# Kernel optimization log

Measured on AMD Instinct MI355X. Metric: run time of the kernel, lower is better.

Reference implementation:

```python
import jax, jax.numpy as jnp
import numpy as np
import math

N_HEADS = 4
N_KV_GROUPS = 1
HEAD_DIM = 256
SLIDING_WINDOW = 512
ROPE_BASE = 1000000.0
EPS = 1e-6


def _rmsnorm(x, gamma):
    # normalize over last dim (head_dim), torch nn.RMSNorm semantics
    ms = jnp.mean(jnp.square(x), axis=-1, keepdims=True)
    return x * jax.lax.rsqrt(ms + EPS) * gamma


def _rope_tables(T, head_dim, dtype):
    inv_freq = 1.0 / (ROPE_BASE ** (jnp.arange(0, head_dim, 2, dtype=jnp.float32) / head_dim))
    t = jnp.arange(T, dtype=jnp.float32)
    freqs = jnp.outer(t, inv_freq)          # [T, head_dim/2]
    return jnp.cos(freqs).astype(dtype), jnp.sin(freqs).astype(dtype)


def _apply_rope(x, cos, sin):
    # x: [B, T, H, hd]; cos/sin: [T, hd/2] broadcast as [1, T, 1, hd/2]
    x0 = x[..., 0::2]
    x1 = x[..., 1::2]
    c = cos[None, :, None, :]
    s = sin[None, :, None, :]
    even = x0 * c - x1 * s
    odd = x0 * s + x1 * c
    return jnp.stack((even, odd), axis=-1).reshape(x.shape)


def setup_inputs() -> dict:
    key = jax.random.key(0)
    ks = jax.random.split(key, 5)
    B, T, C = 2, 4096, 1024
    scale = 0.02
    return {
        "x": jax.random.normal(ks[0], (B, T, C), dtype=jnp.float32),
        "Wq": jax.random.normal(ks[1], (C, C), dtype=jnp.float32) * scale,
        "Wk": jax.random.normal(ks[2], (N_KV_GROUPS * HEAD_DIM, C), dtype=jnp.float32) * scale,
        "Wv": jax.random.normal(ks[3], (N_KV_GROUPS * HEAD_DIM, C), dtype=jnp.float32) * scale,
        "Wo": jax.random.normal(ks[4], (C, C), dtype=jnp.float32) * scale,
        "q_gamma": jnp.ones((HEAD_DIM,), dtype=jnp.float32),
        "k_gamma": jnp.ones((HEAD_DIM,), dtype=jnp.float32),
    }


def reference(x, Wq, Wk, Wv, Wo, q_gamma, k_gamma):
    B, T, C = x.shape
    H, G, hd = N_HEADS, N_KV_GROUPS, HEAD_DIM
    rep = H // G

    q = (x @ Wq.T).reshape(B, T, H, hd)
    k = (x @ Wk.T).reshape(B, T, G, hd)
    v = (x @ Wv.T).reshape(B, T, G, hd)

    q = _rmsnorm(q, q_gamma)
    k = _rmsnorm(k, k_gamma)

    cos, sin = _rope_tables(T, hd, q.dtype)
    q = _apply_rope(q, cos, sin)
    k = _apply_rope(k, cos, sin)

    q = q.transpose(0, 2, 1, 3)                 # [B, H, T, hd]
    k = k.transpose(0, 2, 1, 3)                 # [B, G, T, hd]
    v = v.transpose(0, 2, 1, 3)
    k = jnp.repeat(k, rep, axis=1)              # [B, H, T, hd]
    v = jnp.repeat(v, rep, axis=1)

    scores = jnp.einsum("bhqd,bhkd->bhqk", q, k) / math.sqrt(hd)
    i = jnp.arange(T)[:, None]
    j = jnp.arange(T)[None, :]
    allowed = (j <= i) & (j >= i - SLIDING_WINDOW)   # causal sliding window
    scores = jnp.where(allowed, scores, -jnp.inf)
    attn = jax.nn.softmax(scores, axis=-1)
    out = jnp.einsum("bhqk,bhkd->bhqd", attn, v)     # [B, H, T, hd]
    out = out.transpose(0, 2, 1, 3).reshape(B, T, C)
    return out @ Wo.T
```

## Files before the change

kernel.cpp:

```cpp
#include <hip/hip_runtime.h>
#include <cstdint>
#include <cstddef>

#define T_SEQ 4096
#define NB    2
#define CDIM  1024
#define HD    256
#define NH    4

typedef __attribute__((ext_vector_type(8))) __bf16 bf16x8;
typedef __attribute__((ext_vector_type(4))) __bf16 bf16x4;
typedef __attribute__((ext_vector_type(4))) float  floatx4;

__device__ __forceinline__ floatx4 mfma16(bf16x8 a, bf16x8 b, floatx4 c) {
  return __builtin_amdgcn_mfma_f32_16x16x32_bf16(a, b, c, 0, 0, 0);
}

__device__ __forceinline__ void gl2lds16(const void* g, void* l) {
  __builtin_amdgcn_global_load_lds(
      (__attribute__((address_space(1))) void*)g,
      (__attribute__((address_space(3))) void*)l, 16, 0, 0);
}

__global__ void cvt_f32_bf16(const float* __restrict__ in,
                             __bf16* __restrict__ out, int n4) {
  int i = blockIdx.x * 256 + threadIdx.x;
  if (i < n4) {
    float4 v = ((const float4*)in)[i];
    bf16x4 o;
    o[0] = (__bf16)v.x; o[1] = (__bf16)v.y; o[2] = (__bf16)v.z; o[3] = (__bf16)v.w;
    *(bf16x4*)&out[(size_t)i * 4] = o;
  }
}

template <typename OutT>
__global__ __launch_bounds__(256) void gemm_bt(const __bf16* __restrict__ A,
                                               const __bf16* __restrict__ B,
                                               OutT* __restrict__ C,
                                               int M, int N, int K) {
  __shared__ __bf16 As[128 * 64];
  __shared__ __bf16 Bs[128 * 64];
  const int tid  = threadIdx.x;
  const int lane = tid & 63;
  const int wave = tid >> 6;
  const int wm = wave >> 1, wn = wave & 1;
  const int lrow = lane & 15, quad = lane >> 4;
  const int bm = blockIdx.y, bn = blockIdx.x;

  const __bf16* gA = A + (size_t)(bm * 128) * K;
  const __bf16* gB = B + (size_t)(bn * 128) * K;
  const int arow = tid >> 3;
  const int acol = ((tid & 7) ^ ((tid >> 3) & 7)) * 8;
  const int l7 = lrow & 7;

  floatx4 acc[4][4] = {};

  for (int kt = 0; kt < K; kt += 64) {
#pragma unroll
    for (int i = 0; i < 4; ++i)
      gl2lds16(gA + (size_t)(i * 32 + arow) * K + kt + acol, &As[i * 2048 + tid * 8]);
#pragma unroll
    for (int i = 0; i < 4; ++i)
      gl2lds16(gB + (size_t)(i * 32 + arow) * K + kt + acol, &Bs[i * 2048 + tid * 8]);
    __syncthreads();
#pragma unroll
    for (int kk = 0; kk < 2; ++kk) {
      bf16x8 af[4], bfr[4];
#pragma unroll
      for (int mi = 0; mi < 4; ++mi)
        af[mi] = *(const bf16x8*)&As[(wm * 64 + mi * 16 + lrow) * 64 +
                                     ((kk * 4 + quad) ^ l7) * 8];
#pragma unroll
      for (int ni = 0; ni < 4; ++ni)
        bfr[ni] = *(const bf16x8*)&Bs[(wn * 64 + ni * 16 + lrow) * 64 +
                                      ((kk * 4 + quad) ^ l7) * 8];
#pragma unroll
      for (int mi = 0; mi < 4; ++mi)
#pragma unroll
        for (int ni = 0; ni < 4; ++ni)
          acc[mi][ni] = mfma16(af[mi], bfr[ni], acc[mi][ni]);
    }
    __syncthreads();
  }

  const int row0 = bm * 128 + wm * 64;
  const int col0 = bn * 128 + wn * 64;
#pragma unroll
  for (int mi = 0; mi < 4; ++mi)
#pragma unroll
    for (int ni = 0; ni < 4; ++ni)
#pragma unroll
      for (int r = 0; r < 4; ++r) {
        int row = row0 + mi * 16 + quad * 4 + r;
        int col = col0 + ni * 16 + lrow;
        C[(size_t)row * N + col] = (OutT)acc[mi][ni][r];
      }
}

__global__ __launch_bounds__(256) void rmsrope(const __bf16* __restrict__ qkv,
                                               const float* __restrict__ qg,
                                               const float* __restrict__ kg,
                                               __bf16* __restrict__ qr,
                                               __bf16* __restrict__ kr,
                                               __bf16* __restrict__ vt) {
  __shared__ __bf16 Ls[64 * 256];
  if (blockIdx.x >= 10240) {
    const int vb = blockIdx.x - 10240;
    const int b = vb >> 6, tt = vb & 63;
    const int tid = threadIdx.x;
    const __bf16* src = qkv + ((size_t)(b * 4096 + tt * 64)) * 1536 + 1280;
#pragma unroll
    for (int i = 0; i < 8; ++i)
      gl2lds16(src + (size_t)(i * 8 + (tid >> 5)) * 1536 + (tid & 31) * 8,
               &Ls[i * 2048 + tid * 8]);
    __syncthreads();
    __bf16 buf[64];
#pragma unroll
    for (int i = 0; i < 64; ++i) buf[i] = Ls[i * 256 + tid];
    __bf16* dst = vt + ((size_t)(b * 256 + tid)) * T_SEQ + tt * 64;
#pragma unroll
    for (int i = 0; i < 8; ++i)
      *(bf16x8*)&dst[i * 8] = *(const bf16x8*)&buf[i * 8];
    return;
  }

  const int inst = blockIdx.x * 4 + (threadIdx.x >> 6);
  const int lane = threadIdx.x & 63;
  const int row = inst / 5, which = inst - row * 5;
  const int b = row >> 12, t = row & 4095;

  const int srcoff = (which < 4) ? which * 256 : 1024;
  const __bf16* src = qkv + (size_t)row * 1536 + srcoff;
  bf16x4 xv = *(const bf16x4*)&src[lane * 4];

  float x0 = (float)xv[0], x1 = (float)xv[1], x2 = (float)xv[2], x3 = (float)xv[3];
  float ss = x0 * x0 + x1 * x1 + x2 * x2 + x3 * x3;
#pragma unroll
  for (int off = 32; off >= 1; off >>= 1) ss += __shfl_xor(ss, off);
  const float rms = rsqrtf(ss * (1.0f / 256.0f) + 1e-6f);

  const float* g = (which < 4) ? qg : kg;
  const float4 gv = *(const float4*)&g[lane * 4];
  float y0 = x0 * rms * gv.x, y1 = x1 * rms * gv.y;
  float y2 = x2 * rms * gv.z, y3 = x3 * rms * gv.w;

  const float c_log2 = -19.931568569324174f / 128.0f;
  int p0 = lane * 2, p1 = lane * 2 + 1;
  float a0 = (float)t * exp2f((float)p0 * c_log2);
  float a1 = (float)t * exp2f((float)p1 * c_log2);
  float s0, c0, s1, c1;
  sincosf(a0, &s0, &c0);
  sincosf(a1, &s1, &c1);
  bf16x4 ov;
  ov[0] = (__bf16)(y0 * c0 - y1 * s0);
  ov[1] = (__bf16)(y0 * s0 + y1 * c0);
  ov[2] = (__bf16)(y2 * c1 - y3 * s1);
  ov[3] = (__bf16)(y2 * s1 + y3 * c1);

  __bf16* dst = (which < 4)
      ? qr + ((size_t)((b * NH + which) * T_SEQ) + t) * 256
      : kr + ((size_t)(b * T_SEQ) + t) * 256;
  *(bf16x4*)&dst[lane * 4] = ov;
}

__global__ __launch_bounds__(256, 1) void attn(const __bf16* __restrict__ qr,
                                               const __bf16* __restrict__ kr,
                                               const __bf16* __restrict__ vt,
                                               __bf16* __restrict__ ao) {
  __shared__ __bf16 Ks[2][64 * 256];
  __shared__ __bf16 Vs[2][256 * 64];
  __shared__ __bf16 Ps[4][32 * 64];

  const int bid = blockIdx.x;
  const int qt = bid & 31, h = (bid >> 5) & 3, b = bid >> 7;
  const int tid = threadIdx.x, wave = tid >> 6, lane = tid & 63;
  const int lrow = lane & 15, quad = lane >> 4;
  const int l7 = lrow & 7;

  const __bf16* Q = qr + (size_t)((b * NH + h) * T_SEQ) * 256;
  const __bf16* K = kr + (size_t)(b * T_SEQ) * 256;
  const __bf16* V = vt + (size_t)(b * 256) * T_SEQ;

  const int qbase = qt * 128 + wave * 32;

  bf16x8 qf[2][8];
#pragma unroll
  for (int mt = 0; mt < 2; ++mt)
#pragma unroll
    for (int c = 0; c < 8; ++c)
      qf[mt][c] = *(const bf16x8*)&Q[(size_t)(qbase + mt * 16 + lrow) * 256 +
                                     c * 32 + quad * 8];

  bf16x8 onesv;
#pragma unroll
  for (int j = 0; j < 8; ++j) onesv[j] = (__bf16)1.0f;

  floatx4 o[2][16] = {};
  floatx4 lm[2] = {};

  const int jt0 = (qt >= 4) ? 2 * qt - 8 : 0;
  const int jt1 = 2 * qt + 1;

  {
    const int sel = jt0 & 1;
    const __bf16* Kt = K + (size_t)(jt0 * 64) * 256;
#pragma unroll
    for (int i = 0; i < 8; ++i)
      gl2lds16(Kt + (size_t)(i * 8 + (tid >> 5)) * 256 +
                   ((tid & 31) ^ ((tid >> 5) & 7)) * 8,
               &Ks[sel][i * 2048 + tid * 8]);
#pragma unroll
    for (int i = 0; i < 8; ++i)
      gl2lds16(V + (size_t)(i * 32 + (tid >> 3)) * T_SEQ + jt0 * 64 +
                   ((tid & 7) ^ ((tid >> 3) & 7)) * 8,
               &Vs[sel][i * 2048 + tid * 8]);
  }

  for (int jt = jt0; jt <= jt1; ++jt) {
    __syncthreads();

    if (jt < jt1) {
      const int sel = (jt + 1) & 1;
      const __bf16* Kt = K + (size_t)((jt + 1) * 64) * 256;
#pragma unroll
      for (int i = 0; i < 8; ++i)
        gl2lds16(Kt + (size_t)(i * 8 + (tid >> 5)) * 256 +
                     ((tid & 31) ^ ((tid >> 5) & 7)) * 8,
                 &Ks[sel][i * 2048 + tid * 8]);
#pragma unroll
      for (int i = 0; i < 8; ++i)
        gl2lds16(V + (size_t)(i * 32 + (tid >> 3)) * T_SEQ + (jt + 1) * 64 +
                     ((tid & 7) ^ ((tid >> 3) & 7)) * 8,
                 &Vs[sel][i * 2048 + tid * 8]);
    }

    const __bf16* Kb = Ks[jt & 1];
    const __bf16* Vb = Vs[jt & 1];

    floatx4 s[4][2] = {};
#pragma unroll
    for (int c = 0; c < 8; ++c)
#pragma unroll
      for (int kt16 = 0; kt16 < 4; ++kt16) {
        bf16x8 kf = *(const bf16x8*)&Kb[(kt16 * 16 + lrow) * 256 +
                                        ((c * 4 + quad) ^ l7) * 8];
#pragma unroll
        for (int mt = 0; mt < 2; ++mt)
          s[kt16][mt] = mfma16(kf, qf[mt][c], s[kt16][mt]);
      }

    const bool full = (jt * 64 + 63 <= qt * 128) &&
                      (jt * 64 >= qt * 128 + 127 - 512);

    const float C1 = 0.09016844005556021f;
    const float C2 = 23.083120654223415f;
    __bf16* Pw = &Ps[wave][0];
#pragma unroll
    for (int mt = 0; mt < 2; ++mt)
#pragma unroll
      for (int kt16 = 0; kt16 < 4; ++kt16) {
        bf16x4 pk;
#pragma unroll
        for (int r = 0; r < 4; ++r) {
          float v = s[kt16][mt][r];
          if (!full) {
            const int jk = jt * 64 + kt16 * 16 + quad * 4 + r;
            const int iq = qbase + mt * 16 + lrow;
            v = ((jk <= iq) && (jk + 512 >= iq)) ? v : -1e30f;
          }
          pk[r] = (__bf16)exp2f(v * C1 - C2);
        }
        const int row = mt * 16 + lrow;
        const int chunk = (kt16 * 2 + (quad >> 1)) ^ l7;
        *(bf16x4*)((char*)Pw + row * 128 + chunk * 16 + (quad & 1) * 8) = pk;
      }
    asm volatile("s_waitcnt lgkmcnt(0)" ::: "memory");

    bf16x8 pf[2][2];
#pragma unroll
    for (int mt = 0; mt < 2; ++mt)
#pragma unroll
      for (int kc = 0; kc < 2; ++kc)
        pf[mt][kc] = *(const bf16x8*)((char*)Pw + (mt * 16 + lrow) * 128 +
                                      ((kc * 4 + quad) ^ l7) * 16);

#pragma unroll
    for (int mt = 0; mt < 2; ++mt) {
      lm[mt] = mfma16(pf[mt][0], onesv, lm[mt]);
      lm[mt] = mfma16(pf[mt][1], onesv, lm[mt]);
    }

#pragma unroll
    for (int nt2 = 0; nt2 < 16; ++nt2)
#pragma unroll
      for (int kc = 0; kc < 2; ++kc) {
        bf16x8 vf = *(const bf16x8*)&Vb[(nt2 * 16 + lrow) * 64 +
                                        ((kc * 4 + quad) ^ l7) * 8];
        o[0][nt2] = mfma16(pf[0][kc], vf, o[0][nt2]);
        o[1][nt2] = mfma16(pf[1][kc], vf, o[1][nt2]);
      }
  }

#pragma unroll
  for (int mt = 0; mt < 2; ++mt)
#pragma unroll
    for (int r = 0; r < 4; ++r) {
      const float rl = 1.0f / lm[mt][r];
      const int tg = qbase + mt * 16 + quad * 4 + r;
#pragma unroll
      for (int nt2 = 0; nt2 < 16; ++nt2)
        ao[((size_t)(b * T_SEQ + tg)) * CDIM + h * 256 + nt2 * 16 + lrow] =
            (__bf16)(o[mt][nt2][r] * rl);
    }
}

extern "C" void kernel_launch(void* const* d_in, const int* in_sizes, int n_in,
                              void* d_out, int out_size, void* d_ws, size_t ws_size,
                              hipStream_t stream) {
  const float* x  = (const float*)d_in[0];
  const float* Wq = (const float*)d_in[1];
  const float* Wk = (const float*)d_in[2];
  const float* Wv = (const float*)d_in[3];
  const float* Wo = (const float*)d_in[4];
  const float* qg = (const float*)d_in[5];
  const float* kg = (const float*)d_in[6];
  float* out = (float*)d_out;

  const size_t M = (size_t)NB * T_SEQ;
  char* ws = (char*)d_ws;
  __bf16* xb  = (__bf16*)ws; ws += M * CDIM * 2;
  __bf16* wb  = (__bf16*)ws; ws += (size_t)1536 * CDIM * 2;
  __bf16* wob = (__bf16*)ws; ws += (size_t)CDIM * CDIM * 2;
  __bf16* qkv = (__bf16*)ws; ws += M * 1536 * 2;
  __bf16* qr  = (__bf16*)ws; ws += M * CDIM * 2;
  __bf16* kr  = (__bf16*)ws; ws += M * HD * 2;
  __bf16* vt  = (__bf16*)ws; ws += M * HD * 2;
  __bf16* ao  = (__bf16*)ws;

  cvt_f32_bf16<<<8192, 256, 0, stream>>>(x, xb, 2097152);
  cvt_f32_bf16<<<1024, 256, 0, stream>>>(Wq, wb, 262144);
  cvt_f32_bf16<<<256,  256, 0, stream>>>(Wk, wb + 1024 * 1024, 65536);
  cvt_f32_bf16<<<256,  256, 0, stream>>>(Wv, wb + 1280 * 1024, 65536);
  cvt_f32_bf16<<<1024, 256, 0, stream>>>(Wo, wob, 262144);

  gemm_bt<__bf16><<<dim3(12, 64), 256, 0, stream>>>(xb, wb, qkv, 8192, 1536, 1024);

  rmsrope<<<10368, 256, 0, stream>>>(qkv, qg, kg, qr, kr, vt);

  attn<<<NB * NH * (T_SEQ / 128), 256, 0, stream>>>(qr, kr, vt, ao);

  gemm_bt<float><<<dim3(8, 64), 256, 0, stream>>>(ao, wob, out, 8192, 1024, 1024);
}
```

Baseline: 234.1 us.

## Split attention into 64-query tiles with 2x2 wave split and direct global V reads

The attention kernel now uses 64-query blocks, doubling the grid. Each block's four waves are split two by two: by query half, and by key half for QK^T or output-dim half for PV. V tiles are read straight from global memory instead of being staged in LDS, and K goes from double to single buffering. That frees LDS and allows two blocks per CU through launch bounds. The aim is higher occupancy and better latency hiding, at the cost of more redundant sliding-window tile work per query, an extra barrier per tile and less prefetch overlap.

```diff
diff --git a/kernel.cpp b/kernel.cpp
--- a/kernel.cpp
+++ b/kernel.cpp
@@ -163,17 +163,17 @@
   *(bf16x4*)&dst[lane * 4] = ov;
 }
 
-__global__ __launch_bounds__(256, 1) void attn(const __bf16* __restrict__ qr,
+__global__ __launch_bounds__(256, 2) void attn(const __bf16* __restrict__ qr,
                                                const __bf16* __restrict__ kr,
                                                const __bf16* __restrict__ vt,
                                                __bf16* __restrict__ ao) {
-  __shared__ __bf16 Ks[2][64 * 256];
-  __shared__ __bf16 Vs[2][256 * 64];
-  __shared__ __bf16 Ps[4][32 * 64];
+  __shared__ __bf16 Ks[64 * 256];
+  __shared__ __bf16 Ps[64 * 64];
 
   const int bid = blockIdx.x;
-  const int qt = bid & 31, h = (bid >> 5) & 3, b = bid >> 7;
+  const int qi = bid & 63, h = (bid >> 6) & 3, b = bid >> 8;
   const int tid = threadIdx.x, wave = tid >> 6, lane = tid & 63;
+  const int wq = wave & 1, wk = wave >> 1;
   const int lrow = lane & 15, quad = lane >> 4;
   const int l7 = lrow & 7;
 
@@ -181,136 +181,121 @@
   const __bf16* K = kr + (size_t)(b * T_SEQ) * 256;
   const __bf16* V = vt + (size_t)(b * 256) * T_SEQ;
 
-  const int qbase = qt * 128 + wave * 32;
+  const int qbase = qi * 64;
 
   bf16x8 qf[2][8];
 #pragma unroll
-  for (int mt = 0; mt < 2; ++mt)
+  for (int qt = 0; qt < 2; ++qt)
 #pragma unroll
     for (int c = 0; c < 8; ++c)
-      qf[mt][c] = *(const bf16x8*)&Q[(size_t)(qbase + mt * 16 + lrow) * 256 +
+      qf[qt][c] = *(const bf16x8*)&Q[(size_t)(qbase + wq * 32 + qt * 16 + lrow) * 256 +
                                      c * 32 + quad * 8];
 
   bf16x8 onesv;
 #pragma unroll
   for (int j = 0; j < 8; ++j) onesv[j] = (__bf16)1.0f;
 
-  floatx4 o[2][16] = {};
+  floatx4 o[2][8] = {};
   floatx4 lm[2] = {};
 
-  const int jt0 = (qt >= 4) ? 2 * qt - 8 : 0;
-  const int jt1 = 2 * qt + 1;
+  const int jt0 = (qi >= 8) ? qi - 8 : 0;
+  const int jt1 = qi;
 
   {
-    const int sel = jt0 & 1;
     const __bf16* Kt = K + (size_t)(jt0 * 64) * 256;
 #pragma unroll
     for (int i = 0; i < 8; ++i)
       gl2lds16(Kt + (size_t)(i * 8 + (tid >> 5)) * 256 +
                    ((tid & 31) ^ ((tid >> 5) & 7)) * 8,
-               &Ks[sel][i * 2048 + tid * 8]);
-#pragma unroll
-    for (int i = 0; i < 8; ++i)
-      gl2lds16(V + (size_t)(i * 32 + (tid >> 3)) * T_SEQ + jt0 * 64 +
-                   ((tid & 7) ^ ((tid >> 3) & 7)) * 8,
-               &Vs[sel][i * 2048 + tid * 8]);
+               &Ks[i * 2048 + tid * 8]);
   }
 
   for (int jt = jt0; jt <= jt1; ++jt) {
     __syncthreads();
 
-    if (jt < jt1) {
-      const int sel = (jt + 1) & 1;
-      const __bf16* Kt = K + (size_t)((jt + 1) * 64) * 256;
-#pragma unroll
-      for (int i = 0; i < 8; ++i)
-        gl2lds16(Kt + (size_t)(i * 8 + (tid >> 5)) * 256 +
-                     ((tid & 31) ^ ((tid >> 5) & 7)) * 8,
-                 &Ks[sel][i * 2048 + tid * 8]);
-#pragma unroll
-      for (int i = 0; i < 8; ++i)
-        gl2lds16(V + (size_t)(i * 32 + (tid >> 3)) * T_SEQ + (jt + 1) * 64 +
-                     ((tid & 7) ^ ((tid >> 3) & 7)) * 8,
-                 &Vs[sel][i * 2048 + tid * 8]);
-    }
-
-    const __bf16* Kb = Ks[jt & 1];
-    const __bf16* Vb = Vs[jt & 1];
-
-    floatx4 s[4][2] = {};
+    floatx4 s[2][2] = {};
 #pragma unroll
     for (int c = 0; c < 8; ++c)
 #pragma unroll
-      for (int kt16 = 0; kt16 < 4; ++kt16) {
-        bf16x8 kf = *(const bf16x8*)&Kb[(kt16 * 16 + lrow) * 256 +
+      for (int k16 = 0; k16 < 2; ++k16) {
+        bf16x8 kf = *(const bf16x8*)&Ks[(wk * 32 + k16 * 16 + lrow) * 256 +
                                         ((c * 4 + quad) ^ l7) * 8];
 #pragma unroll
-        for (int mt = 0; mt < 2; ++mt)
-          s[kt16][mt] = mfma16(kf, qf[mt][c], s[kt16][mt]);
-      }
-
-    const bool full = (jt * 64 + 63 <= qt * 128) &&
-                      (jt * 64 >= qt * 128 + 127 - 512);
+        for (int qt = 0; qt < 2; ++qt)
+          s[k16][qt] = mfma16(kf, qf[qt][c], s[k16][qt]);
+      }
+
+    const bool full = (jt < qi) && (jt >= qi - 7);
 
     const float C1 = 0.09016844005556021f;
     const float C2 = 23.083120654223415f;
-    __bf16* Pw = &Ps[wave][0];
-#pragma unroll
-    for (int mt = 0; mt < 2; ++mt)
-#pragma unroll
-      for (int kt16 = 0; kt16 < 4; ++kt16) {
+#pragma unroll
+    for (int k16 = 0; k16 < 2; ++k16)
+#pragma unroll
+      for (int qt = 0; qt < 2; ++qt) {
         bf16x4 pk;
 #pragma unroll
         for (int r = 0; r < 4; ++r) {
-          float v = s[kt16][mt][r];
+          float v = s[k16][qt][r];
           if (!full) {
-            const int jk = jt * 64 + kt16 * 16 + quad * 4 + r;
-            const int iq = qbase + mt * 16 + lrow;
+            const int jk = jt * 64 + wk * 32 + k16 * 16 + quad * 4 + r;
+            const int iq = qbase + wq * 32 + qt * 16 + lrow;
             v = ((jk <= iq) && (jk + 512 >= iq)) ? v : -1e30f;
           }
           pk[r] = (__bf16)exp2f(v * C1 - C2);
         }
-        const int row = mt * 16 + lrow;
-        const int chunk = (kt16 * 2 + (quad >> 1)) ^ l7;
-        *(bf16x4*)((char*)Pw + row * 128 + chunk * 16 + (quad & 1) * 8) = pk;
-      }
-    asm volatile("s_waitcnt lgkmcnt(0)" ::: "memory");
+        const int q = wq * 32 + qt * 16 + lrow;
+        const int chunk = (wk * 4 + k16 * 2 + (quad >> 1)) ^ l7;
+        *(bf16x4*)((char*)Ps + q * 128 + chunk * 16 + (quad & 1) * 8) = pk;
+      }
+    __syncthreads();
+
+    if (jt < jt1) {
+      const __bf16* Kt = K + (size_t)((jt + 1) * 64) * 256;
+#pragma unroll
+      for (int i = 0; i < 8; ++i)
+        gl2lds16(Kt + (size_t)(i * 8 + (tid >> 5)) * 256 +
+                     ((tid & 31) ^ ((tid >> 5) & 7)) * 8,
+                 &Ks[i * 2048 + tid * 8]);
+    }
 
     bf16x8 pf[2][2];
 #pragma unroll
-    for (int mt = 0; mt < 2; ++mt)
-#pragma unroll
-      for (int kc = 0; kc < 2; ++kc)
-        pf[mt][kc] = *(const bf16x8*)((char*)Pw + (mt * 16 + lrow) * 128 +
+    for (int qt = 0; qt < 2; ++qt)
+#pragma unroll
+      for (int kc = 0; kc < 2; ++kc) {
+        const int q = wq * 32 + qt * 16 + lrow;
+        pf[qt][kc] = *(const bf16x8*)((char*)Ps + q * 128 +
                                       ((kc * 4 + quad) ^ l7) * 16);
-
-#pragma unroll
-    for (int mt = 0; mt < 2; ++mt) {
-      lm[mt] = mfma16(pf[mt][0], onesv, lm[mt]);
-      lm[mt] = mfma16(pf[mt][1], onesv, lm[mt]);
+      }
+
+#pragma unroll
+    for (int qt = 0; qt < 2; ++qt) {
+      lm[qt] = mfma16(pf[qt][0], onesv, lm[qt]);
+      lm[qt] = mfma16(pf[qt][1], onesv, lm[qt]);
     }
 
 #pragma unroll
-    for (int nt2 = 0; nt2 < 16; ++nt2)
+    for (int n = 0; n < 8; ++n)
 #pragma unroll
       for (int kc = 0; kc < 2; ++kc) {
-        bf16x8 vf = *(const bf16x8*)&Vb[(nt2 * 16 + lrow) * 64 +
-                                        ((kc * 4 + quad) ^ l7) * 8];
-        o[0][nt2] = mfma16(pf[0][kc], vf, o[0][nt2]);
-        o[1][nt2] = mfma16(pf[1][kc], vf, o[1][nt2]);
-      }
-  }
-
-#pragma unroll
-  for (int mt = 0; mt < 2; ++mt)
+        bf16x8 vf = *(const bf16x8*)&V[(size_t)(wk * 128 + n * 16 + lrow) * T_SEQ +
+                                       jt * 64 + kc * 32 + quad * 8];
+        o[0][n] = mfma16(pf[0][kc], vf, o[0][n]);
+        o[1][n] = mfma16(pf[1][kc], vf, o[1][n]);
+      }
+  }
+
+#pragma unroll
+  for (int qt = 0; qt < 2; ++qt)
 #pragma unroll
     for (int r = 0; r < 4; ++r) {
-      const float rl = 1.0f / lm[mt][r];
-      const int tg = qbase + mt * 16 + quad * 4 + r;
-#pragma unroll
-      for (int nt2 = 0; nt2 < 16; ++nt2)
-        ao[((size_t)(b * T_SEQ + tg)) * CDIM + h * 256 + nt2 * 16 + lrow] =
-            (__bf16)(o[mt][nt2][r] * rl);
+      const float rl = 1.0f / lm[qt][r];
+      const int tg = qbase + wq * 32 + qt * 16 + quad * 4 + r;
+#pragma unroll
+      for (int n = 0; n < 8; ++n)
+        ao[((size_t)(b * T_SEQ + tg)) * CDIM + h * 256 + wk * 128 + n * 16 + lrow] =
+            (__bf16)(o[qt][n][r] * rl);
     }
 }
 
@@ -347,7 +332,7 @@
 
   rmsrope<<<10368, 256, 0, stream>>>(qkv, qg, kg, qr, kr, vt);
 
-  attn<<<NB * NH * (T_SEQ / 128), 256, 0, stream>>>(qr, kr, vt, ao);
+  attn<<<NB * NH * (T_SEQ / 64), 256, 0, stream>>>(qr, kr, vt, ao);
 
   gemm_bt<float><<<dim3(8, 64), 256, 0, stream>>>(ao, wob, out, 8192, 1024, 1024);
 }
```

Result: no change. 235.8 us (+0.8%).
